# Kernel optimization log

Measured on AMD Instinct MI355X. Metric: run time of the kernel, lower is better.

Reference implementation:

```python
import math
import jax, jax.numpy as jnp
import numpy as np

B, D = 64, 768
MAX_V, MAX_D, MAX_A, MAX_T = 512, 256, 128, 64
HEAD_SIZE = D // 12  # 64
SCALE = math.sqrt(HEAD_SIZE)


def make_pad_shifted_mask(input_mask, max_v, max_t, memory_len=0):
    # input_mask: (N, L) with L == memory_len + max_v + max_t
    N, L = input_mask.shape
    sm = jnp.zeros((max_v + max_t, L), input_mask.dtype)
    sm = sm.at[:, :memory_len + max_v].set(1.0)
    sm = sm.at[max_v:, memory_len + max_v:].set(
        jnp.tril(jnp.ones((max_t, max_t), input_mask.dtype)))
    return sm[None] * input_mask[:, None, :]  # (N, max_v+max_t, L)


def make_pad_shifted_mask_case2(mask, v1, v2, t):
    # mask: (N, v2 + t)
    sm = jnp.zeros((v1 + t, v2 + t), mask.dtype)
    sm = sm.at[:, :v2].set(1.0)
    sm = sm.at[v1:, v2:].set(jnp.tril(jnp.ones((t, t), mask.dtype)))
    return sm[None] * mask[:, None, :]  # (N, v1+t, v2+t)


def cross_attention(h1, h2, m1, m2, l1, l2):
    if l1 == l2:
        a12 = make_pad_shifted_mask(m2, l1, MAX_T)
        a21 = make_pad_shifted_mask(m1, l2, MAX_T)
    elif l1 > l2:
        a12 = make_pad_shifted_mask_case2(m2, l1, l2, MAX_T)
        a21 = make_pad_shifted_mask(m1, l2, MAX_T, l1 - l2)
    else:
        a12 = make_pad_shifted_mask(m2, l1, MAX_T, l2 - l1)
        a21 = make_pad_shifted_mask_case2(m1, l2, l1, MAX_T)
    a12 = (1.0 - a12) * -10000.0
    a21 = (1.0 - a21) * -10000.0
    s12 = jnp.einsum('bid,bjd->bij', h1, h2) / SCALE
    s21 = jnp.swapaxes(s12, -1, -2)
    p12 = jax.nn.softmax(s12 + a12, axis=-1)
    p21 = jax.nn.softmax(s21 + a21, axis=-1)
    c12 = jnp.einsum('bij,bjd->bid', p12, h2)
    c21 = jnp.einsum('bij,bjd->bid', p21, h1)
    return c12, c21


def setup_inputs() -> dict:
    key = jax.random.key(0)
    ks = jax.random.split(key, 9)
    Lv, Ld, La = MAX_V + MAX_T, MAX_D + MAX_T, MAX_A + MAX_T
    return {
        'video_embeddings': jax.random.normal(ks[0], (B, Lv, D), jnp.float32),
        'attention_mask': jnp.ones((B, Lv), jnp.float32),
        'detect_embeddings': jax.random.normal(ks[1], (B, Ld, D), jnp.float32),
        'attention_mask_det': jnp.ones((B, Ld), jnp.float32),
        'action_embeddings': jax.random.normal(ks[2], (B, La, D), jnp.float32),
        'attention_mask_act': jnp.ones((B, La), jnp.float32),
        'W_vid': jax.random.normal(ks[3], (D, D), jnp.float32) * 0.02,
        'b_vid': jnp.zeros((D,), jnp.float32),
        'W_det': jax.random.normal(ks[4], (D, D), jnp.float32) * 0.02,
        'b_det': jnp.zeros((D,), jnp.float32),
        'W_act': jax.random.normal(ks[5], (D, D), jnp.float32) * 0.02,
        'b_act': jnp.zeros((D,), jnp.float32),
    }


def reference(video_embeddings, attention_mask, detect_embeddings,
              attention_mask_det, action_embeddings, attention_mask_act,
              W_vid, b_vid, W_det, b_det, W_act, b_act):
    vid = video_embeddings @ W_vid.T + b_vid
    det = detect_embeddings @ W_det.T + b_det
    act = action_embeddings @ W_act.T + b_act
    c_vd, c_dv = cross_attention(vid, det, attention_mask, attention_mask_det, MAX_V, MAX_D)
    c_va, c_av = cross_attention(vid, act, attention_mask, attention_mask_act, MAX_V, MAX_A)
    c_ad, c_da = cross_attention(act, det, attention_mask_act, attention_mask_det, MAX_A, MAX_D)
    return (c_vd + c_va, c_dv + c_da, c_av + c_ad)
```

## Files before the change

### kernel.cpp

```cpp
#include <hip/hip_runtime.h>
#include <stdint.h>
#include <stddef.h>

typedef __attribute__((ext_vector_type(8))) short short8;
typedef __attribute__((ext_vector_type(4))) short short4v;
typedef __attribute__((ext_vector_type(4))) float floatx4;

__device__ __forceinline__ short f2bf(float f) {
    union { float f; uint32_t u; } v; v.f = f;
    uint32_t u = v.u + 0x7fffu + ((v.u >> 16) & 1u);
    return (short)(u >> 16);
}

__device__ __forceinline__ void async16(short* lds, const short* g) {
    __builtin_amdgcn_global_load_lds(
        (const __attribute__((address_space(1))) unsigned int*)g,
        (__attribute__((address_space(3))) unsigned int*)lds, 16, 0, 0);
}

__device__ __forceinline__ void stage128x32(short* lds, const short* src, size_t ld, int t) {
    const short* g = src + (size_t)(t >> 2) * ld + (t & 3) * 8;
    async16(lds + t * 8, g);
    async16(lds + 2048 + t * 8, g + 64 * ld);
}

__global__ __launch_bounds__(256) void cast_kernel(const float* __restrict__ src,
                                                   short* __restrict__ dst, int n4) {
    int i = blockIdx.x * blockDim.x + threadIdx.x;
    if (i < n4) {
        float4 v = ((const float4*)src)[i];
        short4v o;
        o.x = f2bf(v.x); o.y = f2bf(v.y); o.z = f2bf(v.z); o.w = f2bf(v.w);
        ((short4v*)dst)[i] = o;
    }
}

__global__ __launch_bounds__(256) void proj_gemm(
    const short* __restrict__ A, const short* __restrict__ W,
    const float* __restrict__ bias,
    short* __restrict__ Y, short* __restrict__ Yt, int L)
{
    __shared__ short As[4096], Bs[4096];
    const int t = threadIdx.x, w = t >> 6, l = t & 63;
    const int wr = (w >> 1) * 64, wc = (w & 1) * 64, lr = l & 15, lq = l >> 4;
    const size_t m0 = (size_t)blockIdx.x * 128;
    const int n0 = blockIdx.y * 128;
    const short* Ab = A + m0 * 768;
    const short* Bb = W + (size_t)n0 * 768;

    floatx4 acc[4][4];
#pragma unroll
    for (int i = 0; i < 4; ++i)
#pragma unroll
        for (int j = 0; j < 4; ++j) acc[i][j] = (floatx4){0.f, 0.f, 0.f, 0.f};

    for (int k0 = 0; k0 < 768; k0 += 32) {
        stage128x32(As, Ab + k0, 768, t);
        stage128x32(Bs, Bb + k0, 768, t);
        __syncthreads();
        short8 af[4], bf[4];
#pragma unroll
        for (int i = 0; i < 4; ++i) af[i] = *(const short8*)(As + (wr + i * 16 + lr) * 32 + lq * 8);
#pragma unroll
        for (int j = 0; j < 4; ++j) bf[j] = *(const short8*)(Bs + (wc + j * 16 + lr) * 32 + lq * 8);
#pragma unroll
        for (int i = 0; i < 4; ++i)
#pragma unroll
            for (int j = 0; j < 4; ++j)
                acc[i][j] = __builtin_amdgcn_mfma_f32_16x16x32_bf16(af[i], bf[j], acc[i][j], 0, 0, 0);
        __syncthreads();
    }

#pragma unroll
    for (int i = 0; i < 4; ++i) {
        const int mb = (int)m0 + wr + i * 16 + lq * 4;
        const int b_ = mb / L, pos = mb - b_ * L;
#pragma unroll
        for (int j = 0; j < 4; ++j) {
            const int n = n0 + wc + j * 16 + lr;
            const float bv = bias[n];
            short4v tv;
#pragma unroll
            for (int r2 = 0; r2 < 4; ++r2) {
                short hv = f2bf(acc[i][j][r2] + bv);
                Y[(size_t)(mb + r2) * 768 + n] = hv;
                tv[r2] = hv;
            }
            *(short4v*)(Yt + ((size_t)b_ * 768 + n) * L + pos) = tv;
        }
    }
}

template<int C>
__global__ __launch_bounds__(512) void fused_sp(
    const short* __restrict__ K,
    const float* __restrict__ mask,
    const short* __restrict__ Q0, int R0, short* __restrict__ P0,
    const short* __restrict__ Q1, int R1, short* __restrict__ P1)
{
    constexpr int NT = C / 16;
    constexpr int NTW = NT / 4;
    __shared__ short Ks[C * 32];
    __shared__ short Qs[64 * 32];
    __shared__ float red[4][64];

    const int t = threadIdx.x, w = t >> 6, l = t & 63;
    const int wr2 = w >> 2;
    const int wc  = w & 3;
    const int lr = l & 15, lq = l >> 4;

    const int b  = blockIdx.z;
    const int pr = blockIdx.y;
    const int R  = pr ? R1 : R0;
    const int m0 = blockIdx.x * 64;
    if (m0 >= R) return;

    const short* Qb = (pr ? Q1 : Q0) + ((size_t)b * R + m0) * 768;
    short*       Pb = (pr ? P1 : P0) + ((size_t)b * R + m0) * C;
    const short* Kb = K + (size_t)b * C * 768;

    floatx4 acc[2][NTW];
#pragma unroll
    for (int i = 0; i < 2; ++i)
#pragma unroll
        for (int j = 0; j < NTW; ++j) acc[i][j] = (floatx4){0.f, 0.f, 0.f, 0.f};

    for (int k0 = 0; k0 < 768; k0 += 32) {
        constexpr int CH = C * 4;
        for (int c = t; c < CH; c += 512)
            async16(Ks + c * 8, Kb + (size_t)(c >> 2) * 768 + k0 + (c & 3) * 8);
        if (t < 256)
            async16(Qs + t * 8, Qb + (size_t)(t >> 2) * 768 + k0 + (t & 3) * 8);
        __syncthreads();

        short8 af[2], bf[NTW];
#pragma unroll
        for (int i = 0; i < 2; ++i)
            af[i] = *(const short8*)(Qs + (wr2 * 32 + i * 16 + lr) * 32 + lq * 8);
#pragma unroll
        for (int j = 0; j < NTW; ++j)
            bf[j] = *(const short8*)(Ks + ((wc * NTW + j) * 16 + lr) * 32 + lq * 8);
#pragma unroll
        for (int i = 0; i < 2; ++i)
#pragma unroll
            for (int j = 0; j < NTW; ++j)
                acc[i][j] = __builtin_amdgcn_mfma_f32_16x16x32_bf16(af[i], bf[j], acc[i][j], 0, 0, 0);
        __syncthreads();
    }

    const int Rm = R - 64, Cm = C - 64;
    float mval[NTW];
#pragma unroll
    for (int j = 0; j < NTW; ++j)
        mval[j] = mask[(size_t)b * C + (wc * NTW + j) * 16 + lr];

#pragma unroll
    for (int i = 0; i < 2; ++i) {
        const int mmb = m0 + wr2 * 32 + i * 16 + lq * 4;
#pragma unroll
        for (int j = 0; j < NTW; ++j) {
            const int n = (wc * NTW + j) * 16 + lr;
#pragma unroll
            for (int r2 = 0; r2 < 4; ++r2) {
                const int mm = mmb + r2;
                const bool allowed = (n < Cm) || ((mm >= Rm) && ((n - Cm) <= (mm - Rm)));
                const float am = allowed ? mval[j] : 0.f;
                acc[i][j][r2] = acc[i][j][r2] * 0.125f + (am - 1.f) * 10000.f;
            }
        }
    }

    float pmax[2][4];
#pragma unroll
    for (int i = 0; i < 2; ++i)
#pragma unroll
        for (int r2 = 0; r2 < 4; ++r2) {
            float m_ = -3.0e38f;
#pragma unroll
            for (int j = 0; j < NTW; ++j) m_ = fmaxf(m_, acc[i][j][r2]);
#pragma unroll
            for (int d = 1; d < 16; d <<= 1) m_ = fmaxf(m_, __shfl_xor(m_, d, 64));
            pmax[i][r2] = m_;
        }
    if (lr == 0) {
#pragma unroll
        for (int i = 0; i < 2; ++i)
#pragma unroll
            for (int r2 = 0; r2 < 4; ++r2)
                red[wc][wr2 * 32 + i * 16 + lq * 4 + r2] = pmax[i][r2];
    }
    __syncthreads();
#pragma unroll
    for (int i = 0; i < 2; ++i)
#pragma unroll
        for (int r2 = 0; r2 < 4; ++r2) {
            const int rr = wr2 * 32 + i * 16 + lq * 4 + r2;
            pmax[i][r2] = fmaxf(fmaxf(red[0][rr], red[1][rr]), fmaxf(red[2][rr], red[3][rr]));
        }
    __syncthreads();

    float psum[2][4];
#pragma unroll
    for (int i = 0; i < 2; ++i)
#pragma unroll
        for (int r2 = 0; r2 < 4; ++r2) {
            float s_ = 0.f;
#pragma unroll
            for (int j = 0; j < NTW; ++j) {
                const float e = __expf(acc[i][j][r2] - pmax[i][r2]);
                acc[i][j][r2] = e;
                s_ += e;
            }
#pragma unroll
            for (int d = 1; d < 16; d <<= 1) s_ += __shfl_xor(s_, d, 64);
            psum[i][r2] = s_;
        }
    if (lr == 0) {
#pragma unroll
        for (int i = 0; i < 2; ++i)
#pragma unroll
            for (int r2 = 0; r2 < 4; ++r2)
                red[wc][wr2 * 32 + i * 16 + lq * 4 + r2] = psum[i][r2];
    }
    __syncthreads();

#pragma unroll
    for (int i = 0; i < 2; ++i)
#pragma unroll
        for (int r2 = 0; r2 < 4; ++r2) {
            const int rr = wr2 * 32 + i * 16 + lq * 4 + r2;
            const float inv = 1.f / (red[0][rr] + red[1][rr] + red[2][rr] + red[3][rr]);
            short* prow = Pb + (size_t)rr * C;
#pragma unroll
            for (int j = 0; j < NTW; ++j)
                prow[(wc * NTW + j) * 16 + lr] = f2bf(acc[i][j][r2] * inv);
        }
}

__global__ __launch_bounds__(256) void pv_gemm(
    const short* __restrict__ P0, const short* __restrict__ Vt0, int C0,
    const short* __restrict__ P1, const short* __restrict__ Vt1, int C1,
    float* __restrict__ O, int R)
{
    __shared__ short As[4096], Bs[4096];
    const int t = threadIdx.x, w = t >> 6, l = t & 63;
    const int wr = (w >> 1) * 64, wc = (w & 1) * 64, lr = l & 15, lq = l >> 4;
    const int b = blockIdx.z;
    const int m0 = blockIdx.x * 128, n0 = blockIdx.y * 128;

    floatx4 acc[4][4];
#pragma unroll
    for (int i = 0; i < 4; ++i)
#pragma unroll
        for (int j = 0; j < 4; ++j) acc[i][j] = (floatx4){0.f, 0.f, 0.f, 0.f};

    for (int s = 0; s < 2; ++s) {
        const short* Ab = (s ? P1 : P0);
        const short* Bb = (s ? Vt1 : Vt0);
        const int C = s ? C1 : C0;
        Ab += ((size_t)b * R + m0) * C;
        Bb += ((size_t)b * 768 + n0) * C;
        for (int k0 = 0; k0 < C; k0 += 32) {
            stage128x32(As, Ab + k0, C, t);
            stage128x32(Bs, Bb + k0, C, t);
            __syncthreads();
            short8 af[4], bf[4];
#pragma unroll
            for (int i = 0; i < 4; ++i) af[i] = *(const short8*)(As + (wr + i * 16 + lr) * 32 + lq * 8);
#pragma unroll
            for (int j = 0; j < 4; ++j) bf[j] = *(const short8*)(Bs + (wc + j * 16 + lr) * 32 + lq * 8);
#pragma unroll
            for (int i = 0; i < 4; ++i)
#pragma unroll
                for (int j = 0; j < 4; ++j)
                    acc[i][j] = __builtin_amdgcn_mfma_f32_16x16x32_bf16(af[i], bf[j], acc[i][j], 0, 0, 0);
            __syncthreads();
        }
    }

#pragma unroll
    for (int i = 0; i < 4; ++i) {
        const int mb = m0 + wr + i * 16 + lq * 4;
#pragma unroll
        for (int j = 0; j < 4; ++j) {
            const int n = n0 + wc + j * 16 + lr;
#pragma unroll
            for (int r2 = 0; r2 < 4; ++r2) {
                if (mb + r2 < R)
                    O[((size_t)b * R + mb + r2) * 768 + n] = acc[i][j][r2];
            }
        }
    }
}

extern "C" void kernel_launch(void* const* d_in, const int* in_sizes, int n_in,
                              void* d_out, int out_size, void* d_ws, size_t ws_size,
                              hipStream_t stream) {
    const float* vidX = (const float*)d_in[0];
    const float* mV   = (const float*)d_in[1];
    const float* detX = (const float*)d_in[2];
    const float* mD   = (const float*)d_in[3];
    const float* actX = (const float*)d_in[4];
    const float* mA   = (const float*)d_in[5];
    const float* Wv   = (const float*)d_in[6];
    const float* bv   = (const float*)d_in[7];
    const float* Wd   = (const float*)d_in[8];
    const float* bd   = (const float*)d_in[9];
    const float* Wa   = (const float*)d_in[10];
    const float* ba   = (const float*)d_in[11];

    const size_t EV = 28311552, ED = 15728640, EA = 9437184;
    char* p = (char*)d_ws;
    auto alloc = [&](size_t bytes) { char* r = p; p += (bytes + 255) & ~255ULL; return r; };

    short* Wvb = (short*)alloc(589824 * 2);
    short* Wdb = (short*)alloc(589824 * 2);
    short* Wab = (short*)alloc(589824 * 2);
    short* Yv  = (short*)alloc(EV * 2);
    short* Yd  = (short*)alloc(ED * 2);
    short* Ya  = (short*)alloc(EA * 2);
    short* Ytv = (short*)alloc(EV * 2);
    short* Ytd = (short*)alloc(ED * 2);
    short* Yta = (short*)alloc(EA * 2);
    char* xs  = alloc((EV + ED + EA) * 2);
    short* Xv = (short*)xs;
    short* Xd = Xv + EV;
    short* Xa = Xd + ED;
    short* Pvd = (short*)alloc((size_t)64 * 576 * 320 * 2);
    short* Pva = (short*)alloc((size_t)64 * 576 * 192 * 2);
    short* Pdv = (short*)alloc((size_t)64 * 320 * 576 * 2);
    short* Pda = (short*)alloc((size_t)64 * 320 * 192 * 2);
    short* Pav = (short*)alloc((size_t)64 * 192 * 576 * 2);
    short* Pad = (short*)alloc((size_t)64 * 192 * 320 * 2);
    (void)alloc(262144);

    float* o0 = (float*)d_out;
    float* o1 = o0 + EV;
    float* o2 = o1 + ED;

    cast_kernel<<<576, 256, 0, stream>>>(Wv, Wvb, 147456);
    cast_kernel<<<576, 256, 0, stream>>>(Wd, Wdb, 147456);
    cast_kernel<<<576, 256, 0, stream>>>(Wa, Wab, 147456);
    cast_kernel<<<27648, 256, 0, stream>>>(vidX, Xv, (int)(EV / 4));
    cast_kernel<<<15360, 256, 0, stream>>>(detX, Xd, (int)(ED / 4));
    cast_kernel<<<9216, 256, 0, stream>>>(actX, Xa, (int)(EA / 4));

    proj_gemm<<<dim3(288, 6), 256, 0, stream>>>(Xv, Wvb, bv, Yv, Ytv, 576);
    proj_gemm<<<dim3(160, 6), 256, 0, stream>>>(Xd, Wdb, bd, Yd, Ytd, 320);
    proj_gemm<<<dim3(96, 6), 256, 0, stream>>>(Xa, Wab, ba, Ya, Yta, 192);

    fused_sp<576><<<dim3(5, 2, 64), 512, 0, stream>>>(Yv, mV, Yd, 320, Pdv, Ya, 192, Pav);
    fused_sp<320><<<dim3(9, 2, 64), 512, 0, stream>>>(Yd, mD, Yv, 576, Pvd, Ya, 192, Pad);
    fused_sp<192><<<dim3(9, 2, 64), 512, 0, stream>>>(Ya, mA, Yv, 576, Pva, Yd, 320, Pda);

    pv_gemm<<<dim3(5, 6, 64), 256, 0, stream>>>(Pvd, Ytd, 320, Pva, Yta, 192, o0, 576);
    pv_gemm<<<dim3(3, 6, 64), 256, 0, stream>>>(Pdv, Ytv, 576, Pda, Yta, 192, o1, 320);
    pv_gemm<<<dim3(2, 6, 64), 256, 0, stream>>>(Pav, Ytv, 576, Pad, Ytd, 320, o2, 192);
}
```

Before: 1.080 ms.

## Double-buffer K tiles with XOR swizzle and load Q directly to registers in fused_sp

Changes the score GEMM main loop in fused_sp from single-buffered 32-wide K steps to 64-wide steps with two LDS buffers, so the next K tile is prefetched asynchronously while the current one is computed. The K tile layout in LDS is XOR-swizzled to avoid bank conflicts on fragment reads. Q fragments are loaded straight from global into registers instead of being staged through LDS. LDS usage grows substantially (two C×64 buffers), which may lower occupancy for large C, and register pressure rises from the extra Q fragments.

```diff
diff --git a/kernel.cpp b/kernel.cpp
--- a/kernel.cpp
+++ b/kernel.cpp
@@ -100,8 +100,9 @@
 {
     constexpr int NT = C / 16;
     constexpr int NTW = NT / 4;
-    __shared__ short Ks[C * 32];
-    __shared__ short Qs[64 * 32];
+    constexpr int CHI = C / 64;
+    __shared__ short Ks0[C * 64];
+    __shared__ short Ks1[C * 64];
     __shared__ float red[4][64];
 
     const int t = threadIdx.x, w = t >> 6, l = t & 63;
@@ -125,28 +126,64 @@
 #pragma unroll
         for (int j = 0; j < NTW; ++j) acc[i][j] = (floatx4){0.f, 0.f, 0.f, 0.f};
 
-    for (int k0 = 0; k0 < 768; k0 += 32) {
-        constexpr int CH = C * 4;
-        for (int c = t; c < CH; c += 512)
-            async16(Ks + c * 8, Kb + (size_t)(c >> 2) * 768 + k0 + (c & 3) * 8);
-        if (t < 256)
-            async16(Qs + t * 8, Qb + (size_t)(t >> 2) * 768 + k0 + (t & 3) * 8);
+    short8 q0r[4], q1r[4];
+
+#define STAGEK(buf, kk)                                                         \
+    {                                                                           \
+        _Pragma("unroll")                                                       \
+        for (int ci = 0; ci < CHI; ++ci) {                                      \
+            const int c = t + ci * 512;                                         \
+            const int row = c >> 3;                                             \
+            const int piece = (c & 7) ^ (row & 7);                              \
+            async16((buf) + c * 8, Kb + (size_t)row * 768 + (kk) + piece * 8);  \
+        }                                                                       \
+    }
+#define QLOAD(qr, kk)                                                           \
+    {                                                                           \
+        _Pragma("unroll")                                                       \
+        for (int s = 0; s < 2; ++s)                                             \
+            _Pragma("unroll")                                                   \
+            for (int i = 0; i < 2; ++i)                                         \
+                qr[s * 2 + i] = *(const short8*)(                               \
+                    Qb + (size_t)(wr2 * 32 + i * 16 + lr) * 768 + (kk) +        \
+                    s * 32 + lq * 8);                                           \
+    }
+#define COMPUTE(buf, qr)                                                        \
+    {                                                                           \
+        _Pragma("unroll")                                                       \
+        for (int s = 0; s < 2; ++s) {                                           \
+            short8 bfr[NTW];                                                    \
+            _Pragma("unroll")                                                   \
+            for (int j = 0; j < NTW; ++j) {                                     \
+                const int r = (wc * NTW + j) * 16 + lr;                         \
+                const int slot = (s * 4 + lq) ^ (lr & 7);                       \
+                bfr[j] = *(const short8*)((buf) + (r * 8 + slot) * 8);          \
+            }                                                                   \
+            _Pragma("unroll")                                                   \
+            for (int i = 0; i < 2; ++i)                                         \
+                _Pragma("unroll")                                               \
+                for (int j = 0; j < NTW; ++j)                                   \
+                    acc[i][j] = __builtin_amdgcn_mfma_f32_16x16x32_bf16(        \
+                        qr[s * 2 + i], bfr[j], acc[i][j], 0, 0, 0);             \
+        }                                                                       \
+    }
+
+    STAGEK(Ks0, 0);
+    QLOAD(q0r, 0);
+    __syncthreads();
+
+#pragma unroll 1
+    for (int it = 0; it < 12; it += 2) {
+        if (it + 1 < 12) { STAGEK(Ks1, (it + 1) * 64); QLOAD(q1r, (it + 1) * 64); }
+        COMPUTE(Ks0, q0r);
         __syncthreads();
-
-        short8 af[2], bf[NTW];
-#pragma unroll
-        for (int i = 0; i < 2; ++i)
-            af[i] = *(const short8*)(Qs + (wr2 * 32 + i * 16 + lr) * 32 + lq * 8);
-#pragma unroll
-        for (int j = 0; j < NTW; ++j)
-            bf[j] = *(const short8*)(Ks + ((wc * NTW + j) * 16 + lr) * 32 + lq * 8);
-#pragma unroll
-        for (int i = 0; i < 2; ++i)
-#pragma unroll
-            for (int j = 0; j < NTW; ++j)
-                acc[i][j] = __builtin_amdgcn_mfma_f32_16x16x32_bf16(af[i], bf[j], acc[i][j], 0, 0, 0);
+        if (it + 2 < 12) { STAGEK(Ks0, (it + 2) * 64); QLOAD(q0r, (it + 2) * 64); }
+        COMPUTE(Ks1, q1r);
         __syncthreads();
     }
+#undef STAGEK
+#undef QLOAD
+#undef COMPUTE
 
     const int Rm = R - 64, Cm = C - 64;
     float mval[NTW];
```

Result: no change. 1.097 ms (+1.5%).

## Pipeline fused score-softmax kernel with triple-buffered K and concatenated query rows

Applied to the files above, without the earlier changes.

Restructures the fused score+softmax kernel so each block handles 128 rows taken from both query sets concatenated, using 1024 threads. K tiles are staged into three LDS buffers with an XOR swizzle to avoid bank conflicts, and Q fragments are loaded directly from global into registers and double-buffered. Explicit vmcnt waits and raw barriers replace the per-iteration __syncthreads pairs. The aim is to overlap global loads with MFMA work and to cut the wasted blocks that early-returned. The cost is more LDS per block, higher register pressure, and more complex indexing to map rows back to the two outputs.

```diff
diff --git a/kernel.cpp b/kernel.cpp
--- a/kernel.cpp
+++ b/kernel.cpp
@@ -16,6 +16,16 @@
     __builtin_amdgcn_global_load_lds(
         (const __attribute__((address_space(1))) unsigned int*)g,
         (__attribute__((address_space(3))) unsigned int*)lds, 16, 0, 0);
+}
+
+template<int N> __device__ __forceinline__ void vmwait() {
+    if constexpr (N == 0) asm volatile("s_waitcnt vmcnt(0)" ::: "memory");
+    else if constexpr (N == 1) asm volatile("s_waitcnt vmcnt(1)" ::: "memory");
+    else if constexpr (N == 2) asm volatile("s_waitcnt vmcnt(2)" ::: "memory");
+    else if constexpr (N == 3) asm volatile("s_waitcnt vmcnt(3)" ::: "memory");
+    else if constexpr (N == 4) asm volatile("s_waitcnt vmcnt(4)" ::: "memory");
+    else if constexpr (N == 5) asm volatile("s_waitcnt vmcnt(5)" ::: "memory");
+    else if constexpr (N == 6) asm volatile("s_waitcnt vmcnt(6)" ::: "memory");
 }
 
 __device__ __forceinline__ void stage128x32(short* lds, const short* src, size_t ld, int t) {
@@ -91,84 +101,145 @@
     }
 }
 
-template<int C>
-__global__ __launch_bounds__(512) void fused_sp(
+template<int C, int R0, int R1>
+__global__ __launch_bounds__(1024, 4) void fused_sp(
     const short* __restrict__ K,
     const float* __restrict__ mask,
-    const short* __restrict__ Q0, int R0, short* __restrict__ P0,
-    const short* __restrict__ Q1, int R1, short* __restrict__ P1)
+    const short* __restrict__ Q0, short* __restrict__ P0,
+    const short* __restrict__ Q1, short* __restrict__ P1)
 {
     constexpr int NT = C / 16;
     constexpr int NTW = NT / 4;
-    __shared__ short Ks[C * 32];
-    __shared__ short Qs[64 * 32];
-    __shared__ float red[4][64];
+    constexpr int CH = C * 4;
+    constexpr int FULL = CH / 1024;
+    constexpr int REMW = (CH - FULL * 1024) / 16;
+    constexpr int SC = FULL + (REMW ? 1 : 0);
+    constexpr int WN = SC + 2;
+    static_assert((R0 + R1) % 128 == 0, "concat rows must tile by 128");
+
+    __shared__ short Kb0[C * 32], Kb1[C * 32], Kb2[C * 32];
+    __shared__ float red[4][128];
 
     const int t = threadIdx.x, w = t >> 6, l = t & 63;
-    const int wr2 = w >> 2;
+    const int wr4 = w >> 2;
     const int wc  = w & 3;
     const int lr = l & 15, lq = l >> 4;
-
     const int b  = blockIdx.z;
-    const int pr = blockIdx.y;
-    const int R  = pr ? R1 : R0;
-    const int m0 = blockIdx.x * 64;
-    if (m0 >= R) return;
-
-    const short* Qb = (pr ? Q1 : Q0) + ((size_t)b * R + m0) * 768;
-    short*       Pb = (pr ? P1 : P0) + ((size_t)b * R + m0) * C;
+    const int m0 = blockIdx.x * 128;
+
     const short* Kb = K + (size_t)b * C * 768;
 
+    const short* qp[2];
+#pragma unroll
+    for (int i = 0; i < 2; ++i) {
+        const int row = m0 + wr4 * 32 + i * 16 + lr;
+        qp[i] = (row < R0) ? (Q0 + ((size_t)b * R0 + row) * 768)
+                           : (Q1 + ((size_t)b * R1 + (row - R0)) * 768);
+    }
+
     floatx4 acc[2][NTW];
 #pragma unroll
     for (int i = 0; i < 2; ++i)
 #pragma unroll
         for (int j = 0; j < NTW; ++j) acc[i][j] = (floatx4){0.f, 0.f, 0.f, 0.f};
 
-    for (int k0 = 0; k0 < 768; k0 += 32) {
-        constexpr int CH = C * 4;
-        for (int c = t; c < CH; c += 512)
-            async16(Ks + c * 8, Kb + (size_t)(c >> 2) * 768 + k0 + (c & 3) * 8);
-        if (t < 256)
-            async16(Qs + t * 8, Qb + (size_t)(t >> 2) * 768 + k0 + (t & 3) * 8);
-        __syncthreads();
-
-        short8 af[2], bf[NTW];
-#pragma unroll
-        for (int i = 0; i < 2; ++i)
-            af[i] = *(const short8*)(Qs + (wr2 * 32 + i * 16 + lr) * 32 + lq * 8);
-#pragma unroll
-        for (int j = 0; j < NTW; ++j)
-            bf[j] = *(const short8*)(Ks + ((wc * NTW + j) * 16 + lr) * 32 + lq * 8);
-#pragma unroll
-        for (int i = 0; i < 2; ++i)
-#pragma unroll
-            for (int j = 0; j < NTW; ++j)
-                acc[i][j] = __builtin_amdgcn_mfma_f32_16x16x32_bf16(af[i], bf[j], acc[i][j], 0, 0, 0);
-        __syncthreads();
-    }
-
-    const int Rm = R - 64, Cm = C - 64;
+    short8 q0[2], q1[2];
+
+#define STAGEK(buf, kk)                                                          \
+    {                                                                            \
+        _Pragma("unroll")                                                        \
+        for (int ci = 0; ci < FULL; ++ci) {                                      \
+            const int c = t + ci * 1024;                                         \
+            const int row = c >> 2;                                              \
+            const int piece = (c & 3) ^ ((row >> 1) & 3);                        \
+            async16((buf) + c * 8, Kb + (size_t)row * 768 + (kk) + piece * 8);   \
+        }                                                                        \
+        if (REMW) {                                                              \
+            const int c = FULL * 1024 + w * REMW + l;                            \
+            if (l < REMW) {                                                      \
+                const int row = c >> 2;                                          \
+                const int piece = (c & 3) ^ ((row >> 1) & 3);                    \
+                async16((buf) + c * 8, Kb + (size_t)row * 768 + (kk) + piece * 8); \
+            }                                                                    \
+        }                                                                        \
+    }
+
+#define QLOAD(qr, kk)                                                            \
+    {                                                                            \
+        _Pragma("unroll")                                                        \
+        for (int i = 0; i < 2; ++i)                                              \
+            qr[i] = *(const short8*)(qp[i] + (kk) + lq * 8);                     \
+    }
+
+#define COMPUTE(buf, qr)                                                         \
+    {                                                                            \
+        short8 bfr[NTW];                                                         \
+        _Pragma("unroll")                                                        \
+        for (int j = 0; j < NTW; ++j) {                                          \
+            const int r = (wc * NTW + j) * 16 + lr;                              \
+            const int slot = lq ^ ((lr >> 1) & 3);                               \
+            bfr[j] = *(const short8*)((buf) + r * 32 + slot * 8);                \
+        }                                                                        \
+        _Pragma("unroll")                                                        \
+        for (int i = 0; i < 2; ++i)                                              \
+            _Pragma("unroll")                                                    \
+            for (int j = 0; j < NTW; ++j)                                        \
+                acc[i][j] = __builtin_amdgcn_mfma_f32_16x16x32_bf16(             \
+                    qr[i], bfr[j], acc[i][j], 0, 0, 0);                          \
+    }
+
+#define PHASE(p, BC, BS, QU, QN)                                                 \
+    {                                                                            \
+        if constexpr ((p) + 1 < 24) QLOAD(QN, ((p) + 1) * 32);                   \
+        vmwait<((p) == 23) ? 0 : WN>();                                          \
+        __builtin_amdgcn_s_barrier();                                            \
+        __builtin_amdgcn_sched_barrier(0);                                       \
+        if constexpr ((p) + 2 < 24) STAGEK(BS, ((p) + 2) * 32);                  \
+        COMPUTE(BC, QU);                                                         \
+    }
+
+#define PH6(P)                                                                   \
+    PHASE(P + 0, Kb0, Kb2, q0, q1)                                               \
+    PHASE(P + 1, Kb1, Kb0, q1, q0)                                               \
+    PHASE(P + 2, Kb2, Kb1, q0, q1)                                               \
+    PHASE(P + 3, Kb0, Kb2, q1, q0)                                               \
+    PHASE(P + 4, Kb1, Kb0, q0, q1)                                               \
+    PHASE(P + 5, Kb2, Kb1, q1, q0)
+
+    STAGEK(Kb0, 0);
+    QLOAD(q0, 0);
+    STAGEK(Kb1, 32);
+
+    PH6(0) PH6(6) PH6(12) PH6(18)
+
+#undef STAGEK
+#undef QLOAD
+#undef COMPUTE
+#undef PHASE
+#undef PH6
+
+    constexpr int Cm = C - 64;
     float mval[NTW];
 #pragma unroll
     for (int j = 0; j < NTW; ++j)
         mval[j] = mask[(size_t)b * C + (wc * NTW + j) * 16 + lr];
 
 #pragma unroll
-    for (int i = 0; i < 2; ++i) {
-        const int mmb = m0 + wr2 * 32 + i * 16 + lq * 4;
-#pragma unroll
-        for (int j = 0; j < NTW; ++j) {
-            const int n = (wc * NTW + j) * 16 + lr;
-#pragma unroll
-            for (int r2 = 0; r2 < 4; ++r2) {
-                const int mm = mmb + r2;
-                const bool allowed = (n < Cm) || ((mm >= Rm) && ((n - Cm) <= (mm - Rm)));
+    for (int i = 0; i < 2; ++i)
+#pragma unroll
+        for (int r2 = 0; r2 < 4; ++r2) {
+            const int rrl = wr4 * 32 + i * 16 + lq * 4 + r2;
+            const int glob = m0 + rrl;
+            const int lm = (glob < R0) ? glob : glob - R0;
+            const int Rm = ((glob < R0) ? R0 : R1) - 64;
+#pragma unroll
+            for (int j = 0; j < NTW; ++j) {
+                const int n = (wc * NTW + j) * 16 + lr;
+                const bool allowed = (n < Cm) || ((lm >= Rm) && ((n - Cm) <= (lm - Rm)));
                 const float am = allowed ? mval[j] : 0.f;
                 acc[i][j][r2] = acc[i][j][r2] * 0.125f + (am - 1.f) * 10000.f;
             }
         }
-    }
 
     float pmax[2][4];
 #pragma unroll
@@ -182,19 +253,20 @@
             for (int d = 1; d < 16; d <<= 1) m_ = fmaxf(m_, __shfl_xor(m_, d, 64));
             pmax[i][r2] = m_;
         }
+    __syncthreads();
     if (lr == 0) {
 #pragma unroll
         for (int i = 0; i < 2; ++i)
 #pragma unroll
             for (int r2 = 0; r2 < 4; ++r2)
-                red[wc][wr2 * 32 + i * 16 + lq * 4 + r2] = pmax[i][r2];
+                red[wc][wr4 * 32 + i * 16 + lq * 4 + r2] = pmax[i][r2];
     }
     __syncthreads();
 #pragma unroll
     for (int i = 0; i < 2; ++i)
 #pragma unroll
         for (int r2 = 0; r2 < 4; ++r2) {
-            const int rr = wr2 * 32 + i * 16 + lq * 4 + r2;
+            const int rr = wr4 * 32 + i * 16 + lq * 4 + r2;
             pmax[i][r2] = fmaxf(fmaxf(red[0][rr], red[1][rr]), fmaxf(red[2][rr], red[3][rr]));
         }
     __syncthreads();
@@ -220,7 +292,7 @@
         for (int i = 0; i < 2; ++i)
 #pragma unroll
             for (int r2 = 0; r2 < 4; ++r2)
-                red[wc][wr2 * 32 + i * 16 + lq * 4 + r2] = psum[i][r2];
+                red[wc][wr4 * 32 + i * 16 + lq * 4 + r2] = psum[i][r2];
     }
     __syncthreads();
 
@@ -228,9 +300,11 @@
     for (int i = 0; i < 2; ++i)
 #pragma unroll
         for (int r2 = 0; r2 < 4; ++r2) {
-            const int rr = wr2 * 32 + i * 16 + lq * 4 + r2;
-            const float inv = 1.f / (red[0][rr] + red[1][rr] + red[2][rr] + red[3][rr]);
-            short* prow = Pb + (size_t)rr * C;
+            const int rrl = wr4 * 32 + i * 16 + lq * 4 + r2;
+            const int glob = m0 + rrl;
+            short* prow = (glob < R0) ? (P0 + ((size_t)b * R0 + glob) * C)
+                                      : (P1 + ((size_t)b * R1 + (glob - R0)) * C);
+            const float inv = 1.f / (red[0][rrl] + red[1][rrl] + red[2][rrl] + red[3][rrl]);
 #pragma unroll
             for (int j = 0; j < NTW; ++j)
                 prow[(wc * NTW + j) * 16 + lr] = f2bf(acc[i][j][r2] * inv);
@@ -349,9 +423,9 @@
     proj_gemm<<<dim3(160, 6), 256, 0, stream>>>(Xd, Wdb, bd, Yd, Ytd, 320);
     proj_gemm<<<dim3(96, 6), 256, 0, stream>>>(Xa, Wab, ba, Ya, Yta, 192);
 
-    fused_sp<576><<<dim3(5, 2, 64), 512, 0, stream>>>(Yv, mV, Yd, 320, Pdv, Ya, 192, Pav);
-    fused_sp<320><<<dim3(9, 2, 64), 512, 0, stream>>>(Yd, mD, Yv, 576, Pvd, Ya, 192, Pad);
-    fused_sp<192><<<dim3(9, 2, 64), 512, 0, stream>>>(Ya, mA, Yv, 576, Pva, Yd, 320, Pda);
+    fused_sp<576, 320, 192><<<dim3(4, 1, 64), 1024, 0, stream>>>(Yv, mV, Yd, Pdv, Ya, Pav);
+    fused_sp<320, 576, 192><<<dim3(6, 1, 64), 1024, 0, stream>>>(Yd, mD, Yv, Pvd, Ya, Pad);
+    fused_sp<192, 576, 320><<<dim3(7, 1, 64), 1024, 0, stream>>>(Ya, mA, Yv, Pva, Yd, Pda);
 
     pv_gemm<<<dim3(5, 6, 64), 256, 0, stream>>>(Pvd, Ytd, 320, Pva, Yta, 192, o0, 576);
     pv_gemm<<<dim3(3, 6, 64), 256, 0, stream>>>(Pdv, Ytv, 576, Pda, Yta, 192, o1, 320);
```

Measured after the change: 1.190 ms. 1.1x slower.
